# Kernel optimization log

Hardware: AMD Instinct MI355X
Metric: run time of the kernel (lower is better)

## Reference

```python
import jax, jax.numpy as jnp
import numpy as np

D_MODEL = 1024
NUM_HEADS = 16
D_K = D_MODEL // NUM_HEADS
B, S = 2, 2048


def setup_inputs() -> dict:
    key = jax.random.key(0)
    ks = jax.random.split(key, 11)
    s = 1.0 / np.sqrt(D_MODEL)
    inp = {
        "Q": jax.random.normal(ks[0], (B, S, D_MODEL), jnp.float32),
        "K": jax.random.normal(ks[1], (B, S, D_MODEL), jnp.float32),
        "V": jax.random.normal(ks[2], (B, S, D_MODEL), jnp.float32),
        "Wq": jax.random.uniform(ks[3], (D_MODEL, D_MODEL), jnp.float32, -s, s),
        "bq": jax.random.uniform(ks[4], (D_MODEL,), jnp.float32, -s, s),
        "Wk": jax.random.uniform(ks[5], (D_MODEL, D_MODEL), jnp.float32, -s, s),
        "bk": jax.random.uniform(ks[6], (D_MODEL,), jnp.float32, -s, s),
        "Wv": jax.random.uniform(ks[7], (D_MODEL, D_MODEL), jnp.float32, -s, s),
        "bv": jax.random.uniform(ks[8], (D_MODEL,), jnp.float32, -s, s),
        "Wo": jax.random.uniform(ks[9], (D_MODEL, D_MODEL), jnp.float32, -s, s),
        "bo": jax.random.uniform(ks[10], (D_MODEL,), jnp.float32, -s, s),
    }
    return inp


def _split_heads(x):
    b, s, _ = x.shape
    return x.reshape(b, s, NUM_HEADS, D_K).transpose(0, 2, 1, 3)  # [B,H,S,Dk]


def reference(Q, K, V, Wq, bq, Wk, bk, Wv, bv, Wo, bo):
    q = _split_heads(Q @ Wq.T + bq)
    k = _split_heads(K @ Wk.T + bk)
    v = _split_heads(V @ Wv.T + bv)
    scale = 1.0 / jnp.sqrt(jnp.asarray(D_K, q.dtype))
    scores = jnp.einsum("bhqd,bhkd->bhqk", q, k) * scale  # [B,H,S,S]
    attn = jax.nn.softmax(scores, axis=-1)
    out = jnp.einsum("bhqk,bhkd->bhqd", attn, v)
    out = out.transpose(0, 2, 1, 3).reshape(Q.shape[0], -1, D_MODEL)
    return out @ Wo.T + bo
```

## Files before the change

### kernel.cpp

```cpp
#include <hip/hip_runtime.h>
#include <stdint.h>

typedef __bf16 bf16;
typedef __bf16 bf16x8 __attribute__((ext_vector_type(8)));
typedef float floatx4 __attribute__((ext_vector_type(4)));

#define S_LEN 2048
#define DM 1024
#define NH 16
#define DK 64
#define MTOT 4096

__device__ __forceinline__ void gll16(const void* g, void* l) {
  __builtin_amdgcn_global_load_lds(
      (const __attribute__((address_space(1))) void*)g,
      (__attribute__((address_space(3))) void*)l, 16, 0, 0);
}

__global__ __launch_bounds__(256) void cvt_kernel(
    const float* __restrict__ Wq, const float* __restrict__ Wk, const float* __restrict__ Wv,
    const float* __restrict__ Xq, const float* __restrict__ Xk,
    bf16* __restrict__ wqb, bf16* __restrict__ wkb, bf16* __restrict__ wvb,
    bf16* __restrict__ xqb, bf16* __restrict__ xkb)
{
  const int c = blockIdx.x;
  const float* src; bf16* dst; int off;
  if      (c < 512)  { src = Wq; dst = wqb; off = c; }
  else if (c < 1024) { src = Wk; dst = wkb; off = c - 512; }
  else if (c < 1536) { src = Wv; dst = wvb; off = c - 1024; }
  else if (c < 3584) { src = Xq; dst = xqb; off = c - 1536; }
  else               { src = Xk; dst = xkb; off = c - 3584; }
  const size_t base = (size_t)off * 2048 + threadIdx.x * 8;
  float4 a = *(const float4*)(src + base);
  float4 b = *(const float4*)(src + base + 4);
  bf16x8 h;
  h[0] = (bf16)a.x; h[1] = (bf16)a.y; h[2] = (bf16)a.z; h[3] = (bf16)a.w;
  h[4] = (bf16)b.x; h[5] = (bf16)b.y; h[6] = (bf16)b.z; h[7] = (bf16)b.w;
  *(bf16x8*)(dst + base) = h;
}

__global__ __launch_bounds__(256) void proj_kernel(
    const bf16* __restrict__ xqb, const bf16* __restrict__ xkb, const float* __restrict__ Xv,
    const bf16* __restrict__ wqb, const bf16* __restrict__ wkb, const bf16* __restrict__ wvb,
    const float* __restrict__ bqp, const float* __restrict__ bkp, const float* __restrict__ bvp,
    bf16* __restrict__ qb, bf16* __restrict__ kb, bf16* __restrict__ vtb)
{
  const int bid = blockIdx.x;
  const int xcd = bid & 7;
  const int slot = bid >> 3;
  const int m_blk = xcd * 4 + (slot & 3);
  const int n_blk = (slot >> 2) & 7;
  const int z = slot >> 5;

  const bf16* W     = (z == 0) ? wqb : (z == 1) ? wkb : wvb;
  const float* bias = (z == 0) ? bqp : (z == 1) ? bkp : bvp;

  const int m0 = m_blk * 128;
  const int n0 = n_blk * 128;
  const int tid = threadIdx.x;
  const int lane = tid & 63;
  const int wid = tid >> 6;
  const int wm = (wid & 1) * 64;
  const int wn = (wid >> 1) * 64;

  __shared__ unsigned char smemA[32768];
  __shared__ bf16 Bs[128 * 64];
  bf16*  As16 = (bf16*)smemA;
  float* Asf  = (float*)smemA;

  floatx4 acc[4][4];
  #pragma unroll
  for (int i = 0; i < 4; i++)
    #pragma unroll
    for (int j = 0; j < 4; j++) acc[i][j] = (floatx4){0.f, 0.f, 0.f, 0.f};

  const int mr = lane & 15;
  const int q4 = lane >> 4;

  const int r8_in = lane >> 3, cb8_ph = lane & 7;
  const int r4_in = lane >> 4, cb16_ph = lane & 15;

  const bf16* Xb = (z == 0) ? xqb : xkb;

  for (int kt = 0; kt < DM; kt += 64) {
    __syncthreads();
    if (z < 2) {
      #pragma unroll
      for (int j = 0; j < 4; j++) {
        const int c = wid * 4 + j;
        const int row = c * 8 + r8_in;
        const int cb = cb8_ph ^ (row & 7);
        gll16(Xb + (size_t)(m0 + row) * DM + kt + cb * 8, &As16[c * 512]);
      }
    } else {
      #pragma unroll
      for (int j = 0; j < 8; j++) {
        const int c = wid * 8 + j;
        const int row = c * 4 + r4_in;
        const int cb = cb16_ph ^ (row & 7);
        gll16(Xv + (size_t)(m0 + row) * DM + kt + cb * 4, &Asf[c * 256]);
      }
    }
    #pragma unroll
    for (int j = 0; j < 4; j++) {
      const int c = wid * 4 + j;
      const int row = c * 8 + r8_in;
      const int cb = cb8_ph ^ (row & 7);
      gll16(W + (size_t)(n0 + row) * DM + kt + cb * 8, &Bs[c * 512]);
    }
    __syncthreads();

    #pragma unroll
    for (int kk = 0; kk < 2; kk++) {
      bf16x8 af[4], bfr[4];
      #pragma unroll
      for (int mt = 0; mt < 4; mt++) {
        const int row = wm + mt * 16 + mr;
        if (z < 2) {
          const int cb = 4 * kk + q4;
          af[mt] = *(const bf16x8*)&As16[row * 64 + (cb ^ (row & 7)) * 8];
        } else {
          const int cb0 = 8 * kk + 2 * q4;
          const float4 lo = *(const float4*)&Asf[row * 64 + (cb0 ^ (row & 7)) * 4];
          const float4 hi = *(const float4*)&Asf[row * 64 + ((cb0 + 1) ^ (row & 7)) * 4];
          bf16x8 a;
          a[0] = (bf16)lo.x; a[1] = (bf16)lo.y; a[2] = (bf16)lo.z; a[3] = (bf16)lo.w;
          a[4] = (bf16)hi.x; a[5] = (bf16)hi.y; a[6] = (bf16)hi.z; a[7] = (bf16)hi.w;
          af[mt] = a;
        }
      }
      #pragma unroll
      for (int nt = 0; nt < 4; nt++) {
        const int row = wn + nt * 16 + mr;
        const int cb = 4 * kk + q4;
        bfr[nt] = *(const bf16x8*)&Bs[row * 64 + (cb ^ (row & 7)) * 8];
      }
      #pragma unroll
      for (int mt = 0; mt < 4; mt++)
        #pragma unroll
        for (int nt = 0; nt < 4; nt++)
          acc[mt][nt] = __builtin_amdgcn_mfma_f32_16x16x32_bf16(af[mt], bfr[nt], acc[mt][nt], 0, 0, 0);
    }
  }

  const float qscale = (z == 0) ? 0.125f : 1.0f;
  #pragma unroll
  for (int nt = 0; nt < 4; nt++) {
    const int gn = n0 + wn + nt * 16 + mr;
    const float bv = bias[gn];
    const int h = gn >> 6, d = gn & 63;
    #pragma unroll
    for (int mt = 0; mt < 4; mt++) {
      const int mbase = m0 + wm + mt * 16 + q4 * 4;
      #pragma unroll
      for (int r = 0; r < 4; r++) {
        const int gm = mbase + r;
        const int bi = gm >> 11, s = gm & 2047;
        const bf16 hv = (bf16)((acc[mt][nt][r] + bv) * qscale);
        if (z == 2) {
          vtb[(((size_t)(bi * NH + h)) * DK + d) * S_LEN + s] = hv;
        } else if (z == 0) {
          qb[(((size_t)(bi * NH + h)) * S_LEN + s) * DK + d] = hv;
        } else {
          kb[(((size_t)(bi * NH + h)) * S_LEN + s) * DK + d] = hv;
        }
      }
    }
  }
}

__global__ __launch_bounds__(256) void attn_kernel(
    const bf16* __restrict__ qb, const bf16* __restrict__ kb,
    const bf16* __restrict__ vtb, bf16* __restrict__ ob)
{
  const int bid = blockIdx.x;
  const int xcd = bid & 7;
  const int slot = bid >> 3;
  const int bh = xcd * 4 + (slot & 3);
  const int qt = slot >> 2;

  const int tid = threadIdx.x;
  const int lane = tid & 63;
  const int wid = tid >> 6;

  const bf16* qh = qb + (size_t)bh * S_LEN * DK;
  const bf16* kh = kb + (size_t)bh * S_LEN * DK;
  const bf16* vh = vtb + (size_t)bh * DK * S_LEN;

  __shared__ bf16 Ks[128 * 64];
  __shared__ bf16 Vs[64 * 128];
  __shared__ bf16 Ps[4][32][136];

  const int mr = lane & 15;
  const int q4 = lane >> 4;

  bf16x8 aq[2][2];
  #pragma unroll
  for (int mt = 0; mt < 2; mt++)
    #pragma unroll
    for (int kk = 0; kk < 2; kk++)
      aq[mt][kk] = *(const bf16x8*)(qh + (size_t)(qt * 128 + wid * 32 + mt * 16 + mr) * DK + kk * 32 + q4 * 8);

  floatx4 acc_o[2][4];
  #pragma unroll
  for (int mt = 0; mt < 2; mt++)
    #pragma unroll
    for (int dt = 0; dt < 4; dt++) acc_o[mt][dt] = (floatx4){0.f, 0.f, 0.f, 0.f};
  float l_p[2][4] = {{0.f,0.f,0.f,0.f},{0.f,0.f,0.f,0.f}};

  const int r8_in = lane >> 3, cb8_ph = lane & 7;
  const int r4_in = lane >> 4, cb16_ph = lane & 15;

  for (int it = 0; it < S_LEN / 128; it++) {
    const int s0 = it * 128;
    __syncthreads();
    #pragma unroll
    for (int j = 0; j < 4; j++) {
      const int c = wid * 4 + j;
      const int row = c * 8 + r8_in;
      const int cb = cb8_ph ^ (row & 7);
      gll16(kh + (size_t)(s0 + row) * DK + cb * 8, &Ks[c * 512]);
    }
    #pragma unroll
    for (int j = 0; j < 4; j++) {
      const int c = wid * 4 + j;
      const int row = c * 4 + r4_in;
      const int cb = cb16_ph ^ (row & 7);
      gll16(vh + (size_t)row * S_LEN + s0 + cb * 8, &Vs[c * 512]);
    }
    __syncthreads();

    floatx4 sc[2][8];
    #pragma unroll
    for (int mt = 0; mt < 2; mt++)
      #pragma unroll
      for (int i = 0; i < 8; i++) sc[mt][i] = (floatx4){0.f, 0.f, 0.f, 0.f};
    #pragma unroll
    for (int kk = 0; kk < 2; kk++) {
      #pragma unroll
      for (int nt = 0; nt < 8; nt++) {
        const int row = nt * 16 + mr;
        const int cb = kk * 4 + q4;
        bf16x8 b = *(const bf16x8*)&Ks[row * 64 + (cb ^ (row & 7)) * 8];
        #pragma unroll
        for (int mt = 0; mt < 2; mt++)
          sc[mt][nt] = __builtin_amdgcn_mfma_f32_16x16x32_bf16(aq[mt][kk], b, sc[mt][nt], 0, 0, 0);
      }
    }

    #pragma unroll
    for (int mt = 0; mt < 2; mt++)
      #pragma unroll
      for (int nt = 0; nt < 8; nt++)
        #pragma unroll
        for (int r = 0; r < 4; r++) {
          const float pv = __expf(sc[mt][nt][r]);
          l_p[mt][r] += pv;
          Ps[wid][mt * 16 + q4 * 4 + r][nt * 16 + mr] = (bf16)pv;
        }

    #pragma unroll
    for (int kk2 = 0; kk2 < 4; kk2++) {
      bf16x8 ap[2];
      #pragma unroll
      for (int mt = 0; mt < 2; mt++)
        ap[mt] = *(const bf16x8*)&Ps[wid][mt * 16 + mr][kk2 * 32 + q4 * 8];
      #pragma unroll
      for (int dt = 0; dt < 4; dt++) {
        const int row = dt * 16 + mr;
        const int cb = kk2 * 4 + q4;
        bf16x8 b = *(const bf16x8*)&Vs[row * 128 + (cb ^ (row & 7)) * 8];
        #pragma unroll
        for (int mt = 0; mt < 2; mt++)
          acc_o[mt][dt] = __builtin_amdgcn_mfma_f32_16x16x32_bf16(ap[mt], b, acc_o[mt][dt], 0, 0, 0);
      }
    }
  }

  const int bi = bh >> 4, h = bh & 15;
  #pragma unroll
  for (int mt = 0; mt < 2; mt++) {
    float inv[4];
    #pragma unroll
    for (int r = 0; r < 4; r++) {
      float v = l_p[mt][r];
      #pragma unroll
      for (int off = 1; off < 16; off <<= 1) v += __shfl_xor(v, off, 16);
      inv[r] = 1.0f / v;
    }
    #pragma unroll
    for (int dt = 0; dt < 4; dt++) {
      const int d = dt * 16 + mr;
      #pragma unroll
      for (int r = 0; r < 4; r++) {
        const int s = qt * 128 + wid * 32 + mt * 16 + q4 * 4 + r;
        ob[((size_t)(bi * S_LEN + s)) * DM + h * DK + d] = (bf16)(acc_o[mt][dt][r] * inv[r]);
      }
    }
  }
}

__global__ __launch_bounds__(256) void oproj_kernel(
    const bf16* __restrict__ X, const float* __restrict__ W,
    const float* __restrict__ bias, float* __restrict__ out)
{
  const int bid = blockIdx.x;
  const int xcd = bid & 7;
  const int slot = bid >> 3;
  const int m0 = (xcd * 4 + (slot & 3)) * 128;
  const int n0 = (slot >> 2) * 64;

  const int tid = threadIdx.x;
  const int lane = tid & 63;
  const int wid = tid >> 6;
  const int wm = wid * 32;

  __shared__ bf16  As[128 * 64];
  __shared__ float Bsf[64 * 64];

  floatx4 acc[2][4];
  #pragma unroll
  for (int i = 0; i < 2; i++)
    #pragma unroll
    for (int j = 0; j < 4; j++) acc[i][j] = (floatx4){0.f, 0.f, 0.f, 0.f};

  const int mr = lane & 15;
  const int q4 = lane >> 4;

  const int r8_in = lane >> 3, cb8_ph = lane & 7;
  const int r4_in = lane >> 4, cb16_ph = lane & 15;

  for (int kt = 0; kt < DM; kt += 64) {
    __syncthreads();
    #pragma unroll
    for (int j = 0; j < 4; j++) {
      const int c = wid * 4 + j;
      const int row = c * 8 + r8_in;
      const int cb = cb8_ph ^ (row & 7);
      gll16(X + (size_t)(m0 + row) * DM + kt + cb * 8, &As[c * 512]);
    }
    #pragma unroll
    for (int j = 0; j < 4; j++) {
      const int c = wid * 4 + j;
      const int row = c * 4 + r4_in;
      const int cb = cb16_ph ^ (row & 7);
      gll16(W + (size_t)(n0 + row) * DM + kt + cb * 4, &Bsf[c * 256]);
    }
    __syncthreads();

    #pragma unroll
    for (int kk = 0; kk < 2; kk++) {
      bf16x8 af[2], bfr[4];
      #pragma unroll
      for (int mt = 0; mt < 2; mt++) {
        const int row = wm + mt * 16 + mr;
        const int cb = 4 * kk + q4;
        af[mt] = *(const bf16x8*)&As[row * 64 + (cb ^ (row & 7)) * 8];
      }
      #pragma unroll
      for (int nt = 0; nt < 4; nt++) {
        const int row = nt * 16 + mr;
        const int cb0 = 8 * kk + 2 * q4;
        const float4 lo = *(const float4*)&Bsf[row * 64 + (cb0 ^ (row & 7)) * 4];
        const float4 hi = *(const float4*)&Bsf[row * 64 + ((cb0 + 1) ^ (row & 7)) * 4];
        bf16x8 b;
        b[0] = (bf16)lo.x; b[1] = (bf16)lo.y; b[2] = (bf16)lo.z; b[3] = (bf16)lo.w;
        b[4] = (bf16)hi.x; b[5] = (bf16)hi.y; b[6] = (bf16)hi.z; b[7] = (bf16)hi.w;
        bfr[nt] = b;
      }
      #pragma unroll
      for (int mt = 0; mt < 2; mt++)
        #pragma unroll
        for (int nt = 0; nt < 4; nt++)
          acc[mt][nt] = __builtin_amdgcn_mfma_f32_16x16x32_bf16(af[mt], bfr[nt], acc[mt][nt], 0, 0, 0);
    }
  }

  #pragma unroll
  for (int nt = 0; nt < 4; nt++) {
    const int gn = n0 + nt * 16 + mr;
    const float bv = bias[gn];
    #pragma unroll
    for (int mt = 0; mt < 2; mt++) {
      const int mbase = m0 + wm + mt * 16 + q4 * 4;
      #pragma unroll
      for (int r = 0; r < 4; r++)
        out[(size_t)(mbase + r) * DM + gn] = acc[mt][nt][r] + bv;
    }
  }
}

extern "C" void kernel_launch(void* const* d_in, const int* in_sizes, int n_in,
                              void* d_out, int out_size, void* d_ws, size_t ws_size,
                              hipStream_t stream) {
  const float* Q  = (const float*)d_in[0];
  const float* K  = (const float*)d_in[1];
  const float* V  = (const float*)d_in[2];
  const float* Wq = (const float*)d_in[3];
  const float* bq = (const float*)d_in[4];
  const float* Wk = (const float*)d_in[5];
  const float* bk = (const float*)d_in[6];
  const float* Wv = (const float*)d_in[7];
  const float* bv = (const float*)d_in[8];
  const float* Wo = (const float*)d_in[9];
  const float* bo = (const float*)d_in[10];
  float* out = (float*)d_out;

  const size_t NE = (size_t)MTOT * DM;
  bf16* qb  = (bf16*)d_ws;
  bf16* kb  = qb + NE;
  bf16* vtb = kb + NE;
  bf16* ao  = vtb + NE;
  bf16* wqb = ao;
  bf16* wkb = ao + (size_t)DM * DM;
  bf16* wvb = ao + 2 * (size_t)DM * DM;
  bf16* xqb = (bf16*)d_out;
  bf16* xkb = xqb + NE;

  cvt_kernel<<<dim3(5632), 256, 0, stream>>>(Wq, Wk, Wv, Q, K, wqb, wkb, wvb, xqb, xkb);
  proj_kernel<<<dim3(768), 256, 0, stream>>>(xqb, xkb, V, wqb, wkb, wvb, bq, bk, bv, qb, kb, vtb);
  attn_kernel<<<dim3(512), 256, 0, stream>>>(qb, kb, vtb, ao);
  oproj_kernel<<<dim3(512), 256, 0, stream>>>(ao, Wo, bo, out);
}
```

Before: 261.0 us.

## Split QKV projection into QK and V kernels with double-buffered LDS loads

The combined projection kernel is split into a bf16 Q/K kernel and a separate fp32-input V kernel. Each now double-buffers its LDS tiles, issuing the next k-tile's global-to-LDS loads before computing on the current one, with explicit vmcnt waits and raw barriers. This is meant to overlap memory latency with MFMA work and to drop the z-branching. The cost is more LDS per block (64KB in the QK kernel, 96KB in the V kernel), which lowers occupancy, plus one extra kernel launch that serialises the V projection after QK.

Result: faster. 248.5 us (-4.8%).

```diff
diff --git a/kernel.cpp b/kernel.cpp
--- a/kernel.cpp
+++ b/kernel.cpp
@@ -39,11 +39,11 @@
   *(bf16x8*)(dst + base) = h;
 }
 
-__global__ __launch_bounds__(256) void proj_kernel(
-    const bf16* __restrict__ xqb, const bf16* __restrict__ xkb, const float* __restrict__ Xv,
-    const bf16* __restrict__ wqb, const bf16* __restrict__ wkb, const bf16* __restrict__ wvb,
-    const float* __restrict__ bqp, const float* __restrict__ bkp, const float* __restrict__ bvp,
-    bf16* __restrict__ qb, bf16* __restrict__ kb, bf16* __restrict__ vtb)
+__global__ __launch_bounds__(256) void proj_qk_kernel(
+    const bf16* __restrict__ xqb, const bf16* __restrict__ xkb,
+    const bf16* __restrict__ wqb, const bf16* __restrict__ wkb,
+    const float* __restrict__ bqp, const float* __restrict__ bkp,
+    bf16* __restrict__ qb, bf16* __restrict__ kb)
 {
   const int bid = blockIdx.x;
   const int xcd = bid & 7;
@@ -52,8 +52,9 @@
   const int n_blk = (slot >> 2) & 7;
   const int z = slot >> 5;
 
-  const bf16* W     = (z == 0) ? wqb : (z == 1) ? wkb : wvb;
-  const float* bias = (z == 0) ? bqp : (z == 1) ? bkp : bvp;
+  const bf16* X     = z ? xkb : xqb;
+  const bf16* W     = z ? wkb : wqb;
+  const float* bias = z ? bkp : bqp;
 
   const int m0 = m_blk * 128;
   const int n0 = n_blk * 128;
@@ -63,10 +64,8 @@
   const int wm = (wid & 1) * 64;
   const int wn = (wid >> 1) * 64;
 
-  __shared__ unsigned char smemA[32768];
-  __shared__ bf16 Bs[128 * 64];
-  bf16*  As16 = (bf16*)smemA;
-  float* Asf  = (float*)smemA;
+  __shared__ bf16 As[2][128 * 64];
+  __shared__ bf16 Bs[2][128 * 64];
 
   floatx4 acc[4][4];
   #pragma unroll
@@ -76,39 +75,36 @@
 
   const int mr = lane & 15;
   const int q4 = lane >> 4;
-
   const int r8_in = lane >> 3, cb8_ph = lane & 7;
-  const int r4_in = lane >> 4, cb16_ph = lane & 15;
-
-  const bf16* Xb = (z == 0) ? xqb : xkb;
-
+
+  #define STAGE_QK(buf, kt)                                                   \
+    {                                                                         \
+      _Pragma("unroll")                                                       \
+      for (int j = 0; j < 4; j++) {                                           \
+        const int c = wid * 4 + j;                                            \
+        const int row = c * 8 + r8_in;                                        \
+        const int cb = cb8_ph ^ (row & 7);                                    \
+        gll16(X + (size_t)(m0 + row) * DM + (kt) + cb * 8, &As[buf][c * 512]);\
+      }                                                                       \
+      _Pragma("unroll")                                                       \
+      for (int j = 0; j < 4; j++) {                                           \
+        const int c = wid * 4 + j;                                            \
+        const int row = c * 8 + r8_in;                                        \
+        const int cb = cb8_ph ^ (row & 7);                                    \
+        gll16(W + (size_t)(n0 + row) * DM + (kt) + cb * 8, &Bs[buf][c * 512]);\
+      }                                                                       \
+    }
+
+  STAGE_QK(0, 0);
+  int cur = 0;
   for (int kt = 0; kt < DM; kt += 64) {
-    __syncthreads();
-    if (z < 2) {
-      #pragma unroll
-      for (int j = 0; j < 4; j++) {
-        const int c = wid * 4 + j;
-        const int row = c * 8 + r8_in;
-        const int cb = cb8_ph ^ (row & 7);
-        gll16(Xb + (size_t)(m0 + row) * DM + kt + cb * 8, &As16[c * 512]);
-      }
+    if (kt + 64 < DM) {
+      STAGE_QK(cur ^ 1, kt + 64);
+      asm volatile("s_waitcnt vmcnt(8)" ::: "memory");
     } else {
-      #pragma unroll
-      for (int j = 0; j < 8; j++) {
-        const int c = wid * 8 + j;
-        const int row = c * 4 + r4_in;
-        const int cb = cb16_ph ^ (row & 7);
-        gll16(Xv + (size_t)(m0 + row) * DM + kt + cb * 4, &Asf[c * 256]);
-      }
-    }
-    #pragma unroll
-    for (int j = 0; j < 4; j++) {
-      const int c = wid * 4 + j;
-      const int row = c * 8 + r8_in;
-      const int cb = cb8_ph ^ (row & 7);
-      gll16(W + (size_t)(n0 + row) * DM + kt + cb * 8, &Bs[c * 512]);
-    }
-    __syncthreads();
+      asm volatile("s_waitcnt vmcnt(0)" ::: "memory");
+    }
+    __builtin_amdgcn_s_barrier();
 
     #pragma unroll
     for (int kk = 0; kk < 2; kk++) {
@@ -116,24 +112,14 @@
       #pragma unroll
       for (int mt = 0; mt < 4; mt++) {
         const int row = wm + mt * 16 + mr;
-        if (z < 2) {
-          const int cb = 4 * kk + q4;
-          af[mt] = *(const bf16x8*)&As16[row * 64 + (cb ^ (row & 7)) * 8];
-        } else {
-          const int cb0 = 8 * kk + 2 * q4;
-          const float4 lo = *(const float4*)&Asf[row * 64 + (cb0 ^ (row & 7)) * 4];
-          const float4 hi = *(const float4*)&Asf[row * 64 + ((cb0 + 1) ^ (row & 7)) * 4];
-          bf16x8 a;
-          a[0] = (bf16)lo.x; a[1] = (bf16)lo.y; a[2] = (bf16)lo.z; a[3] = (bf16)lo.w;
-          a[4] = (bf16)hi.x; a[5] = (bf16)hi.y; a[6] = (bf16)hi.z; a[7] = (bf16)hi.w;
-          af[mt] = a;
-        }
+        const int cb = 4 * kk + q4;
+        af[mt] = *(const bf16x8*)&As[cur][row * 64 + (cb ^ (row & 7)) * 8];
       }
       #pragma unroll
       for (int nt = 0; nt < 4; nt++) {
         const int row = wn + nt * 16 + mr;
         const int cb = 4 * kk + q4;
-        bfr[nt] = *(const bf16x8*)&Bs[row * 64 + (cb ^ (row & 7)) * 8];
+        bfr[nt] = *(const bf16x8*)&Bs[cur][row * 64 + (cb ^ (row & 7)) * 8];
       }
       #pragma unroll
       for (int mt = 0; mt < 4; mt++)
@@ -141,9 +127,14 @@
         for (int nt = 0; nt < 4; nt++)
           acc[mt][nt] = __builtin_amdgcn_mfma_f32_16x16x32_bf16(af[mt], bfr[nt], acc[mt][nt], 0, 0, 0);
     }
-  }
+
+    __builtin_amdgcn_s_barrier();
+    cur ^= 1;
+  }
+  #undef STAGE_QK
 
   const float qscale = (z == 0) ? 0.125f : 1.0f;
+  bf16* dst = (z == 0) ? qb : kb;
   #pragma unroll
   for (int nt = 0; nt < 4; nt++) {
     const int gn = n0 + wn + nt * 16 + mr;
@@ -157,13 +148,118 @@
         const int gm = mbase + r;
         const int bi = gm >> 11, s = gm & 2047;
         const bf16 hv = (bf16)((acc[mt][nt][r] + bv) * qscale);
-        if (z == 2) {
-          vtb[(((size_t)(bi * NH + h)) * DK + d) * S_LEN + s] = hv;
-        } else if (z == 0) {
-          qb[(((size_t)(bi * NH + h)) * S_LEN + s) * DK + d] = hv;
-        } else {
-          kb[(((size_t)(bi * NH + h)) * S_LEN + s) * DK + d] = hv;
-        }
+        dst[(((size_t)(bi * NH + h)) * S_LEN + s) * DK + d] = hv;
+      }
+    }
+  }
+}
+
+__global__ __launch_bounds__(256) void proj_v_kernel(
+    const float* __restrict__ Xv, const bf16* __restrict__ wvb,
+    const float* __restrict__ bvp, bf16* __restrict__ vtb)
+{
+  const int bid = blockIdx.x;
+  const int xcd = bid & 7;
+  const int slot = bid >> 3;
+  const int m_blk = xcd * 4 + (slot & 3);
+  const int n_blk = slot >> 2;
+
+  const int m0 = m_blk * 128;
+  const int n0 = n_blk * 128;
+  const int tid = threadIdx.x;
+  const int lane = tid & 63;
+  const int wid = tid >> 6;
+  const int wm = (wid & 1) * 64;
+  const int wn = (wid >> 1) * 64;
+
+  __shared__ float Asf[2][128 * 64];
+  __shared__ bf16  Bs[2][128 * 64];
+
+  floatx4 acc[4][4];
+  #pragma unroll
+  for (int i = 0; i < 4; i++)
+    #pragma unroll
+    for (int j = 0; j < 4; j++) acc[i][j] = (floatx4){0.f, 0.f, 0.f, 0.f};
+
+  const int mr = lane & 15;
+  const int q4 = lane >> 4;
+  const int r8_in = lane >> 3, cb8_ph = lane & 7;
+  const int r4_in = lane >> 4, cb16_ph = lane & 15;
+
+  #define STAGE_V(buf, kt)                                                     \
+    {                                                                          \
+      _Pragma("unroll")                                                        \
+      for (int j = 0; j < 8; j++) {                                            \
+        const int c = wid * 8 + j;                                             \
+        const int row = c * 4 + r4_in;                                         \
+        const int cb = cb16_ph ^ (row & 7);                                    \
+        gll16(Xv + (size_t)(m0 + row) * DM + (kt) + cb * 4, &Asf[buf][c * 256]);\
+      }                                                                        \
+      _Pragma("unroll")                                                        \
+      for (int j = 0; j < 4; j++) {                                            \
+        const int c = wid * 4 + j;                                             \
+        const int row = c * 8 + r8_in;                                         \
+        const int cb = cb8_ph ^ (row & 7);                                     \
+        gll16(wvb + (size_t)(n0 + row) * DM + (kt) + cb * 8, &Bs[buf][c * 512]);\
+      }                                                                        \
+    }
+
+  STAGE_V(0, 0);
+  int cur = 0;
+  for (int kt = 0; kt < DM; kt += 64) {
+    if (kt + 64 < DM) {
+      STAGE_V(cur ^ 1, kt + 64);
+      asm volatile("s_waitcnt vmcnt(12)" ::: "memory");
+    } else {
+      asm volatile("s_waitcnt vmcnt(0)" ::: "memory");
+    }
+    __builtin_amdgcn_s_barrier();
+
+    #pragma unroll
+    for (int kk = 0; kk < 2; kk++) {
+      bf16x8 af[4], bfr[4];
+      #pragma unroll
+      for (int mt = 0; mt < 4; mt++) {
+        const int row = wm + mt * 16 + mr;
+        const int cb0 = 8 * kk + 2 * q4;
+        const float4 lo = *(const float4*)&Asf[cur][row * 64 + (cb0 ^ (row & 7)) * 4];
+        const float4 hi = *(const float4*)&Asf[cur][row * 64 + ((cb0 + 1) ^ (row & 7)) * 4];
+        bf16x8 a;
+        a[0] = (bf16)lo.x; a[1] = (bf16)lo.y; a[2] = (bf16)lo.z; a[3] = (bf16)lo.w;
+        a[4] = (bf16)hi.x; a[5] = (bf16)hi.y; a[6] = (bf16)hi.z; a[7] = (bf16)hi.w;
+        af[mt] = a;
+      }
+      #pragma unroll
+      for (int nt = 0; nt < 4; nt++) {
+        const int row = wn + nt * 16 + mr;
+        const int cb = 4 * kk + q4;
+        bfr[nt] = *(const bf16x8*)&Bs[cur][row * 64 + (cb ^ (row & 7)) * 8];
+      }
+      #pragma unroll
+      for (int mt = 0; mt < 4; mt++)
+        #pragma unroll
+        for (int nt = 0; nt < 4; nt++)
+          acc[mt][nt] = __builtin_amdgcn_mfma_f32_16x16x32_bf16(af[mt], bfr[nt], acc[mt][nt], 0, 0, 0);
+    }
+
+    __builtin_amdgcn_s_barrier();
+    cur ^= 1;
+  }
+  #undef STAGE_V
+
+  #pragma unroll
+  for (int nt = 0; nt < 4; nt++) {
+    const int gn = n0 + wn + nt * 16 + mr;
+    const float bv = bvp[gn];
+    const int h = gn >> 6, d = gn & 63;
+    #pragma unroll
+    for (int mt = 0; mt < 4; mt++) {
+      const int mbase = m0 + wm + mt * 16 + q4 * 4;
+      #pragma unroll
+      for (int r = 0; r < 4; r++) {
+        const int gm = mbase + r;
+        const int bi = gm >> 11, s = gm & 2047;
+        vtb[(((size_t)(bi * NH + h)) * DK + d) * S_LEN + s] = (bf16)(acc[mt][nt][r] + bv);
       }
     }
   }
@@ -418,7 +514,8 @@
   bf16* xkb = xqb + NE;
 
   cvt_kernel<<<dim3(5632), 256, 0, stream>>>(Wq, Wk, Wv, Q, K, wqb, wkb, wvb, xqb, xkb);
-  proj_kernel<<<dim3(768), 256, 0, stream>>>(xqb, xkb, V, wqb, wkb, wvb, bq, bk, bv, qb, kb, vtb);
+  proj_qk_kernel<<<dim3(512), 256, 0, stream>>>(xqb, xkb, wqb, wkb, bq, bk, qb, kb);
+  proj_v_kernel<<<dim3(256), 256, 0, stream>>>(V, wvb, bv, vtb);
   attn_kernel<<<dim3(512), 256, 0, stream>>>(qb, kb, vtb, ao);
   oproj_kernel<<<dim3(512), 256, 0, stream>>>(ao, Wo, bo, out);
 }
```
